# Performance work log

Measured on AMD Instinct MI355X. Metric: run time of the kernel, lower is better.

Reference implementation:

```python
import jax, jax.numpy as jnp
import numpy as np

B, N, DIM_IN, DIM_INNER, DIM_OUT, WINDOW = 4, 4096, 1024, 1024, 1024, 128


def setup_inputs() -> dict:
    key = jax.random.key(0)
    k1, k2, k3, k4 = jax.random.split(key, 4)
    x = jax.random.normal(k1, (B, N, DIM_IN), dtype=jnp.float32)
    # to_qkv: Linear(dim_in, 3*dim_inner, bias=False); stored as [in, 3*inner] for x @ W
    w_qkv = jax.random.normal(k2, (DIM_IN, 3 * DIM_INNER), dtype=jnp.float32) / np.sqrt(DIM_IN)
    # to_out: Linear(dim_inner, dim_out) with bias
    w_out = jax.random.normal(k3, (DIM_INNER, DIM_OUT), dtype=jnp.float32) / np.sqrt(DIM_INNER)
    b_out = jax.random.normal(k4, (DIM_OUT,), dtype=jnp.float32) * 0.01
    return {"x": x, "w_qkv": w_qkv, "w_out": w_out, "b_out": b_out}


def reference(x, w_qkv, w_out, b_out):
    b, n, _ = x.shape
    w = WINDOW
    scale = DIM_INNER ** (-0.5)
    # n is a multiple of window, so pad_to_multiple is a no-op
    qkv = jnp.einsum('bnd,de->bne', x, w_qkv)
    q, k, v = jnp.split(qkv, 3, axis=-1)
    nw = n // w
    win = lambda t: t.reshape(b, nw, w, DIM_INNER)  # b (w n) d -> b w n d
    q, k, v = win(q), win(k), win(v)
    # pad one zero block at the front of the window axis
    kp = jnp.pad(k, ((0, 0), (1, 0), (0, 0), (0, 0)))
    # concat previous block + current block along token axis -> (b, nw, 2w, d)
    k2 = jnp.concatenate([kp[:, :-1], kp[:, 1:]], axis=2)
    # NOTE: faithful to source bug: the lambda references k (not t), so v is
    # overwritten with the concatenated k blocks as well.
    v2 = k2
    sim = jnp.einsum('bwid,bwjd->bwij', q, k2) * scale  # (b, nw, w, 2w)
    i, j = w, 2 * w
    mask = jnp.triu(jnp.ones((i, j), dtype=bool), j - i + 1)  # causal within lookback window
    mask_value = -jnp.finfo(sim.dtype).max
    sim = jnp.where(mask[None, None], mask_value, sim)
    attn = jax.nn.softmax(sim, axis=-1)
    out = jnp.einsum('bwij,bwjd->bwid', attn, v2)
    out = out.reshape(b, n, DIM_INNER)[:, :n]
    return jnp.einsum('bnd,de->bne', out, w_out) + b_out
```

## Files before the change

### kernel.cpp

```cpp
#include <hip/hip_runtime.h>
#include <float.h>


#define B_SZ 4
#define SEQ 4096
#define DIM 1024
#define WIN 128
#define NWIN 32
#define TW 256
#define NROWS (B_SZ * SEQ)
#define KPAD 4224

typedef float f32x4 __attribute__((ext_vector_type(4)));
typedef __bf16 bf16x8 __attribute__((ext_vector_type(8)));

__device__ __forceinline__ unsigned short f2b(float f) {
    unsigned int u = __float_as_uint(f);
    u += 0x7FFF + ((u >> 16) & 1);
    return (unsigned short)(u >> 16);
}

__device__ __forceinline__ void gld_lds16(const unsigned short* g, unsigned short* l) {
    __builtin_amdgcn_global_load_lds(
        (const __attribute__((address_space(1))) void*)g,
        (__attribute__((address_space(3))) void*)l, 16, 0, 0);
}

__device__ __forceinline__ void mfma_core(
    const unsigned short* __restrict__ A, int lda,
    const unsigned short* __restrict__ Bt, int ldb, int K,
    unsigned short* As, unsigned short* Bs, f32x4 (&acc)[4][4])
{
    const int tid = threadIdx.x;
    const int wv = tid >> 6, lane = tid & 63;
    const int wr = wv >> 1, wc = wv & 1;

#pragma unroll
    for (int m = 0; m < 4; ++m)
#pragma unroll
        for (int n = 0; n < 4; ++n) acc[m][n] = (f32x4){0.f, 0.f, 0.f, 0.f};

    for (int k0 = 0; k0 < K; k0 += 64) {
#pragma unroll
        for (int it = 0; it < 4; ++it) {
            int rbase = wv * 32 + it * 8;
            const unsigned short* g =
                A + (size_t)(rbase + (lane >> 3)) * lda + k0 + (lane & 7) * 8;
            gld_lds16(g, As + rbase * 64);
        }
#pragma unroll
        for (int it = 0; it < 4; ++it) {
            int rbase = wv * 32 + it * 8;
            const unsigned short* g =
                Bt + (size_t)(rbase + (lane >> 3)) * ldb + k0 + (lane & 7) * 8;
            gld_lds16(g, Bs + rbase * 64);
        }
        __syncthreads();

#pragma unroll
        for (int ks = 0; ks < 2; ++ks) {
            bf16x8 af[4], bfr[4];
            const int kof = ks * 32 + (lane >> 4) * 8;
#pragma unroll
            for (int m = 0; m < 4; ++m)
                af[m] = *(const bf16x8*)(As + (wr * 64 + m * 16 + (lane & 15)) * 64 + kof);
#pragma unroll
            for (int n = 0; n < 4; ++n)
                bfr[n] = *(const bf16x8*)(Bs + (wc * 64 + n * 16 + (lane & 15)) * 64 + kof);
#pragma unroll
            for (int m = 0; m < 4; ++m)
#pragma unroll
                for (int n = 0; n < 4; ++n)
                    acc[m][n] = __builtin_amdgcn_mfma_f32_16x16x32_bf16(
                        af[m], bfr[n], acc[m][n], 0, 0, 0);
        }
        __syncthreads();
    }
}


__global__ __launch_bounds__(256) void k_prep_x(const float* __restrict__ x,
                                                unsigned short* __restrict__ xb)
{
    int i = blockIdx.x * 256 + threadIdx.x;
    float4 a = *(const float4*)&x[(size_t)i * 8];
    float4 b = *(const float4*)&x[(size_t)i * 8 + 4];
    ushort4 lo, hi;
    lo.x = f2b(a.x); lo.y = f2b(a.y); lo.z = f2b(a.z); lo.w = f2b(a.w);
    hi.x = f2b(b.x); hi.y = f2b(b.y); hi.z = f2b(b.z); hi.w = f2b(b.w);
    *(ushort4*)&xb[(size_t)i * 8] = lo;
    *(ushort4*)&xb[(size_t)i * 8 + 4] = hi;
}

__global__ __launch_bounds__(256) void k_transpose(const float* __restrict__ src,
    int src_ld, int col0, int R, unsigned short* __restrict__ dst)
{
    __shared__ float T[32][33];
    const int r0 = blockIdx.y * 32, c0 = blockIdx.x * 32;
    const int cx = threadIdx.x & 31, ry = threadIdx.x >> 5;
#pragma unroll
    for (int i = 0; i < 4; ++i)
        T[ry + 8 * i][cx] = src[(size_t)(r0 + ry + 8 * i) * src_ld + col0 + c0 + cx];
    __syncthreads();
#pragma unroll
    for (int i = 0; i < 4; ++i)
        dst[(size_t)(c0 + ry + 8 * i) * R + r0 + cx] = f2b(T[cx][ry + 8 * i]);
}

__global__ __launch_bounds__(256) void k_zero_kpad(unsigned short* __restrict__ kbuf)
{
    int t = blockIdx.x * 256 + threadIdx.x;
    int b = t >> 14, r = t & 16383;
    float4 z = {0.f, 0.f, 0.f, 0.f};
    *(float4*)&kbuf[(size_t)b * KPAD * DIM + (size_t)r * 8] = z;
}

__global__ __launch_bounds__(256) void k_zero_ktpad(unsigned short* __restrict__ ktr)
{
    int t = blockIdx.x * 256 + threadIdx.x;
    int b = t >> 14, rem = t & 16383;
    int d = rem >> 4, s = rem & 15;
    float4 z = {0.f, 0.f, 0.f, 0.f};
    *(float4*)&ktr[((size_t)b * DIM + d) * KPAD + s * 8] = z;
}

__global__ __launch_bounds__(256) void k_gemm_qk(
    const unsigned short* __restrict__ xb, const unsigned short* __restrict__ wqkvT,
    unsigned short* __restrict__ qbuf, unsigned short* __restrict__ kbuf,
    unsigned short* __restrict__ ktr)
{
    __shared__ unsigned short As[128 * 64], Bs[128 * 64];
    f32x4 acc[4][4];
    const int bm = blockIdx.y * 128, bn = blockIdx.x * 128;
    mfma_core(xb + (size_t)bm * DIM, DIM, wqkvT + (size_t)bn * DIM, DIM, DIM, As, Bs, acc);

    const int tid = threadIdx.x, wv = tid >> 6, lane = tid & 63;
    const int wr = wv >> 1, wc = wv & 1;
#pragma unroll
    for (int m = 0; m < 4; ++m) {
        const int row0 = bm + wr * 64 + m * 16 + (lane >> 4) * 4;
#pragma unroll
        for (int n = 0; n < 4; ++n) {
            const int col = bn + wc * 64 + n * 16 + (lane & 15);
            if (col < DIM) {
#pragma unroll
                for (int r = 0; r < 4; ++r)
                    qbuf[(size_t)(row0 + r) * DIM + col] = f2b(acc[m][n][r]);
            } else {
                const int d = col - DIM;
                const int b = row0 >> 12, tok0 = row0 & 4095;
#pragma unroll
                for (int r = 0; r < 4; ++r)
                    kbuf[((size_t)b * KPAD + 128 + tok0 + r) * DIM + d] = f2b(acc[m][n][r]);
                ushort4 kt;
                kt.x = f2b(acc[m][n][0]); kt.y = f2b(acc[m][n][1]);
                kt.z = f2b(acc[m][n][2]); kt.w = f2b(acc[m][n][3]);
                *(ushort4*)&ktr[((size_t)b * DIM + d) * KPAD + 128 + tok0] = kt;
            }
        }
    }
}

__global__ __launch_bounds__(256) void k_sim(
    const unsigned short* __restrict__ qbuf, const unsigned short* __restrict__ kbuf,
    float* __restrict__ sim)
{
    __shared__ unsigned short As[128 * 64], Bs[128 * 64];
    f32x4 acc[4][4];
    const int win = blockIdx.y, ct = blockIdx.x;
    const int b = win >> 5, w = win & 31;
    const unsigned short* Ap = qbuf + ((size_t)b * SEQ + w * WIN) * DIM;
    const unsigned short* Bp = kbuf + ((size_t)b * KPAD + w * WIN + ct * 128) * DIM;
    mfma_core(Ap, DIM, Bp, DIM, DIM, As, Bs, acc);

    const int tid = threadIdx.x, wv = tid >> 6, lane = tid & 63;
    const int wr = wv >> 1, wc = wv & 1;
    const float scale = 0.03125f;
#pragma unroll
    for (int m = 0; m < 4; ++m) {
        const int qi0 = wr * 64 + m * 16 + (lane >> 4) * 4;
#pragma unroll
        for (int n = 0; n < 4; ++n) {
            const int jc = ct * 128 + wc * 64 + n * 16 + (lane & 15);
#pragma unroll
            for (int r = 0; r < 4; ++r) {
                const int qi = qi0 + r;
                float v = (jc > qi + WIN) ? -FLT_MAX : acc[m][n][r] * scale;
                sim[((size_t)win * WIN + qi) * TW + jc] = v;
            }
        }
    }
}

__global__ __launch_bounds__(256) void k_softmax(const float* __restrict__ sim,
                                                 unsigned short* __restrict__ attnb)
{
    const int row = blockIdx.x * 4 + (threadIdx.x >> 6);
    const int lane = threadIdx.x & 63;
    const float* p = sim + (size_t)row * TW;
    float4 v = *(const float4*)&p[lane * 4];
    float m = fmaxf(fmaxf(v.x, v.y), fmaxf(v.z, v.w));
#pragma unroll
    for (int off = 32; off; off >>= 1) m = fmaxf(m, __shfl_xor(m, off));
    float e0 = expf(v.x - m), e1 = expf(v.y - m);
    float e2 = expf(v.z - m), e3 = expf(v.w - m);
    float s = e0 + e1 + e2 + e3;
#pragma unroll
    for (int off = 32; off; off >>= 1) s += __shfl_xor(s, off);
    float inv = 1.f / s;
    ushort4 o;
    o.x = f2b(e0 * inv); o.y = f2b(e1 * inv); o.z = f2b(e2 * inv); o.w = f2b(e3 * inv);
    *(ushort4*)&attnb[(size_t)row * TW + lane * 4] = o;
}

__global__ __launch_bounds__(256) void k_pv(
    const unsigned short* __restrict__ attnb, const unsigned short* __restrict__ ktr,
    unsigned short* __restrict__ aout)
{
    __shared__ unsigned short As[128 * 64], Bs[128 * 64];
    f32x4 acc[4][4];
    const int win = blockIdx.y, ct = blockIdx.x;
    const int b = win >> 5, w = win & 31;
    const unsigned short* Ap = attnb + (size_t)win * WIN * TW;
    const unsigned short* Bp = ktr + ((size_t)b * DIM + ct * 128) * KPAD + w * WIN;
    mfma_core(Ap, TW, Bp, KPAD, TW, As, Bs, acc);

    const int tid = threadIdx.x, wv = tid >> 6, lane = tid & 63;
    const int wr = wv >> 1, wc = wv & 1;
#pragma unroll
    for (int m = 0; m < 4; ++m) {
        const int row0 = wr * 64 + m * 16 + (lane >> 4) * 4;
#pragma unroll
        for (int n = 0; n < 4; ++n) {
            const int col = ct * 128 + wc * 64 + n * 16 + (lane & 15);
#pragma unroll
            for (int r = 0; r < 4; ++r)
                aout[((size_t)b * SEQ + w * WIN + row0 + r) * DIM + col] =
                    f2b(acc[m][n][r]);
        }
    }
}

__global__ __launch_bounds__(256) void k_out(
    const unsigned short* __restrict__ aout, const unsigned short* __restrict__ woutT,
    const float* __restrict__ bias, float* __restrict__ out)
{
    __shared__ unsigned short As[128 * 64], Bs[128 * 64];
    f32x4 acc[4][4];
    const int bm = blockIdx.y * 128, bn = blockIdx.x * 128;
    mfma_core(aout + (size_t)bm * DIM, DIM, woutT + (size_t)bn * DIM, DIM, DIM, As, Bs, acc);

    const int tid = threadIdx.x, wv = tid >> 6, lane = tid & 63;
    const int wr = wv >> 1, wc = wv & 1;
#pragma unroll
    for (int m = 0; m < 4; ++m) {
        const int row0 = bm + wr * 64 + m * 16 + (lane >> 4) * 4;
#pragma unroll
        for (int n = 0; n < 4; ++n) {
            const int col = bn + wc * 64 + n * 16 + (lane & 15);
            const float bb = bias[col];
#pragma unroll
            for (int r = 0; r < 4; ++r)
                out[(size_t)(row0 + r) * DIM + col] = acc[m][n][r] + bb;
        }
    }
}

extern "C" void kernel_launch(void* const* d_in, const int* in_sizes, int n_in,
                              void* d_out, int out_size, void* d_ws, size_t ws_size,
                              hipStream_t stream)
{
    const float* x     = (const float*)d_in[0];
    const float* w_qkv = (const float*)d_in[1];
    const float* w_out = (const float*)d_in[2];
    const float* b_out = (const float*)d_in[3];
    float* out = (float*)d_out;

    char* p = (char*)d_ws;
    unsigned short* xb    = (unsigned short*)p; p += (size_t)NROWS * DIM * 2;
    unsigned short* wqkvT = (unsigned short*)p; p += (size_t)2 * DIM * DIM * 2;
    unsigned short* woutT = (unsigned short*)p; p += (size_t)DIM * DIM * 2;
    unsigned short* qbuf  = (unsigned short*)p; p += (size_t)NROWS * DIM * 2;
    unsigned short* kbuf  = (unsigned short*)p; p += (size_t)B_SZ * KPAD * DIM * 2;
    unsigned short* ktr   = (unsigned short*)p; p += (size_t)B_SZ * DIM * KPAD * 2;
    float*          simb  = (float*)p;          p += (size_t)NROWS * TW * 4;
    unsigned short* attnb = (unsigned short*)p; p += (size_t)NROWS * TW * 2;
    unsigned short* aout  = (unsigned short*)p; p += (size_t)NROWS * DIM * 2;

    k_prep_x<<<NROWS * DIM / 8 / 256, 256, 0, stream>>>(x, xb);
    k_transpose<<<dim3(2 * DIM / 32, DIM / 32), 256, 0, stream>>>(w_qkv, 3 * DIM, 0, DIM, wqkvT);
    k_transpose<<<dim3(DIM / 32, DIM / 32), 256, 0, stream>>>(w_out, DIM, 0, DIM, woutT);
    k_zero_kpad<<<256, 256, 0, stream>>>(kbuf);
    k_zero_ktpad<<<256, 256, 0, stream>>>(ktr);

    k_gemm_qk<<<dim3(2 * DIM / 128, NROWS / 128), 256, 0, stream>>>(xb, wqkvT, qbuf, kbuf, ktr);
    k_sim<<<dim3(2, B_SZ * NWIN), 256, 0, stream>>>(qbuf, kbuf, simb);
    k_softmax<<<NROWS / 4, 256, 0, stream>>>(simb, attnb);
    k_pv<<<dim3(DIM / 128, B_SZ * NWIN), 256, 0, stream>>>(attnb, ktr, aout);
    k_out<<<dim3(DIM / 128, NROWS / 128), 256, 0, stream>>>(aout, woutT, b_out, out);
}
```

Measured before the change: 364.9 us.

## Use 256x256 double-buffered swizzled MFMA GEMM core for QK and output projections

Adds a new GEMM core that uses 256x256 output tiles with 512 threads, double-buffered LDS filled by direct global-to-LDS loads, XOR-swizzled LDS reads and a phased schedule with explicit waitcnt, barriers and s_setprio. The QK projection and the output projection kernels move to it, with a remapped 1D grid that groups tiles for cache locality. The aim is more data reuse per tile and overlap of global loads with MFMA work in the two largest GEMMs. The cost is 128KB of LDS and a large accumulator per block, which limits occupancy and relies on the hand-tuned wait counts being correct.

```diff
diff --git a/kernel.cpp b/kernel.cpp
--- a/kernel.cpp
+++ b/kernel.cpp
@@ -26,6 +26,114 @@
         (__attribute__((address_space(3))) void*)l, 16, 0, 0);
 }
 
+__device__ __forceinline__ bf16x8 lds_read_swz(const unsigned short* tb, int row, int kbyte) {
+    int L = row * 128 + kbyte;
+    L ^= ((L >> 9) & 1) << 5;
+    return *(const bf16x8*)((const char*)tb + L);
+}
+
+#define BAR __builtin_amdgcn_s_barrier()
+#define PRI1 __builtin_amdgcn_s_setprio(1)
+#define PRI0 __builtin_amdgcn_s_setprio(0)
+#define WAIT_LGKM0 do { asm volatile("s_waitcnt lgkmcnt(0)" ::: "memory"); \
+                        __builtin_amdgcn_sched_barrier(0); } while (0)
+#define WAIT_VM8   do { asm volatile("s_waitcnt vmcnt(8)" ::: "memory");  \
+                        __builtin_amdgcn_sched_barrier(0); } while (0)
+#define WAIT_VM0   do { asm volatile("s_waitcnt vmcnt(0)" ::: "memory");  \
+                        __builtin_amdgcn_sched_barrier(0); } while (0)
+
+#define LDAF(BUF, MH)                                                        \
+    _Pragma("unroll") for (int m_ = 0; m_ < 4; ++m_)                         \
+    _Pragma("unroll") for (int ks_ = 0; ks_ < 2; ++ks_)                      \
+        afq[MH][m_][ks_] = lds_read_swz(bufA[BUF],                           \
+            wr * 128 + (MH) * 64 + m_ * 16 + fr, ks_ * 64 + kby);
+
+#define LDBF(BUF, NH)                                                        \
+    _Pragma("unroll") for (int n_ = 0; n_ < 2; ++n_)                         \
+    _Pragma("unroll") for (int ks_ = 0; ks_ < 2; ++ks_)                      \
+        bfq[n_][ks_] = lds_read_swz(bufB[BUF],                               \
+            wc * 64 + (NH) * 32 + n_ * 16 + fr, ks_ * 64 + kby);
+
+#define MFQ(MH, NH)                                                          \
+    _Pragma("unroll") for (int ks_ = 0; ks_ < 2; ++ks_)                      \
+    _Pragma("unroll") for (int m_ = 0; m_ < 4; ++m_)                         \
+    _Pragma("unroll") for (int n_ = 0; n_ < 2; ++n_)                         \
+        acc[(MH) * 4 + m_][(NH) * 2 + n_] =                                  \
+            __builtin_amdgcn_mfma_f32_16x16x32_bf16(afq[MH][m_][ks_],        \
+                bfq[n_][ks_], acc[(MH) * 4 + m_][(NH) * 2 + n_], 0, 0, 0);
+
+#define STG_A(BUF, HJ, K0) gld_lds16(A + soffA[HJ] + (K0), bufA[BUF] + ldst[HJ])
+#define STG_B(BUF, HJ, K0) gld_lds16(Bt + soffB[HJ] + (K0), bufB[BUF] + ldst[HJ])
+
+#define PHASES03(BUF, KST, ST)                                               \
+    LDAF(BUF, 0); LDBF(BUF, 0);                                              \
+    BAR; WAIT_LGKM0; PRI1; MFQ(0, 0); PRI0; BAR;                             \
+    LDAF(BUF, 1);                                                            \
+    BAR; WAIT_LGKM0; PRI1; MFQ(1, 0); PRI0; BAR;                             \
+    LDBF(BUF, 1);                                                            \
+    if (ST) { STG_A(BUF, 0, KST); STG_A(BUF, 1, KST);                        \
+              STG_A(BUF, 2, KST); STG_A(BUF, 3, KST); }                      \
+    BAR; WAIT_LGKM0; PRI1; MFQ(1, 1); PRI0; BAR;                             \
+    if (ST) { STG_B(BUF, 0, KST); STG_B(BUF, 1, KST);                        \
+              STG_B(BUF, 2, KST); STG_B(BUF, 3, KST); }                      \
+    BAR; WAIT_LGKM0; PRI1; MFQ(0, 1); PRI0;
+
+__device__ __forceinline__ void core256(
+    const unsigned short* __restrict__ A, int lda,
+    const unsigned short* __restrict__ Bt, int ldb, int K,
+    unsigned short* lds, f32x4 (&acc)[8][4],
+    int wid, int lane, int wr, int wc)
+{
+    unsigned short* bufA[2] = { lds, lds + 32768 };
+    unsigned short* bufB[2] = { lds + 16384, lds + 49152 };
+
+    const int kby = (lane >> 4) * 16;
+    const int fr = lane & 15;
+
+    int soffA[4], soffB[4], ldst[4];
+#pragma unroll
+    for (int hj = 0; hj < 4; ++hj) {
+        const int half = hj >> 1, j = hj & 1;
+        const int P = half * 16384 + wid * 2048 + j * 1024 + lane * 16;
+        const int L = P ^ (((P >> 9) & 1) << 5);
+        const int row = L >> 7, col = (L & 127) >> 1;
+        soffA[hj] = row * lda + col;
+        soffB[hj] = row * ldb + col;
+        ldst[hj] = (half * 16384 + wid * 2048 + j * 1024) >> 1;
+    }
+
+    bf16x8 afq[2][4][2], bfq[2][2];
+#pragma unroll
+    for (int m = 0; m < 8; ++m)
+#pragma unroll
+        for (int n = 0; n < 4; ++n) acc[m][n] = (f32x4){0.f, 0.f, 0.f, 0.f};
+
+#pragma unroll
+    for (int hj = 0; hj < 4; ++hj) STG_A(0, hj, 0);
+#pragma unroll
+    for (int hj = 0; hj < 4; ++hj) STG_B(0, hj, 0);
+#pragma unroll
+    for (int hj = 0; hj < 4; ++hj) STG_A(1, hj, 64);
+#pragma unroll
+    for (int hj = 0; hj < 4; ++hj) STG_B(1, hj, 64);
+    WAIT_VM8;
+    BAR;
+
+    const int NITER = K >> 7;
+#pragma unroll 1
+    for (int i = 0; i < NITER; ++i) {
+        const bool st = (i + 1 < NITER);
+        const int ka = (2 * i + 2) * 64;
+        const int kb = (2 * i + 3) * 64;
+        PHASES03(0, ka, st)
+        if (st) { WAIT_VM8; } else { WAIT_VM0; }
+        BAR;
+        PHASES03(1, kb, st)
+        if (st) { WAIT_VM8; }
+        BAR;
+    }
+}
+
 __device__ __forceinline__ void mfma_core(
     const unsigned short* __restrict__ A, int lda,
     const unsigned short* __restrict__ Bt, int ldb, int K,
@@ -77,7 +185,6 @@
         __syncthreads();
     }
 }
-
 
 __global__ __launch_bounds__(256) void k_prep_x(const float* __restrict__ x,
                                                 unsigned short* __restrict__ xb)
@@ -124,24 +231,30 @@
     *(float4*)&ktr[((size_t)b * DIM + d) * KPAD + s * 8] = z;
 }
 
-__global__ __launch_bounds__(256) void k_gemm_qk(
+__global__ __launch_bounds__(512, 2) void k_gemm_qk(
     const unsigned short* __restrict__ xb, const unsigned short* __restrict__ wqkvT,
     unsigned short* __restrict__ qbuf, unsigned short* __restrict__ kbuf,
     unsigned short* __restrict__ ktr)
 {
-    __shared__ unsigned short As[128 * 64], Bs[128 * 64];
-    f32x4 acc[4][4];
-    const int bm = blockIdx.y * 128, bn = blockIdx.x * 128;
-    mfma_core(xb + (size_t)bm * DIM, DIM, wqkvT + (size_t)bn * DIM, DIM, DIM, As, Bs, acc);
-
-    const int tid = threadIdx.x, wv = tid >> 6, lane = tid & 63;
-    const int wr = wv >> 1, wc = wv & 1;
-#pragma unroll
-    for (int m = 0; m < 4; ++m) {
-        const int row0 = bm + wr * 64 + m * 16 + (lane >> 4) * 4;
+    __shared__ unsigned short lds[65536];
+    const int tid = threadIdx.x, wid = tid >> 6, lane = tid & 63;
+    const int wr = wid >> 2, wc = wid & 3;
+    const int wg = blockIdx.x;
+    const int x = (wg & 7) * 64 + (wg >> 3);
+    const int bm = (x & 63) * 256;
+    const int bn = (x >> 6) * 256;
+
+    f32x4 acc[8][4];
+    core256(xb + (size_t)bm * DIM, DIM, wqkvT + (size_t)bn * DIM, DIM, DIM,
+            lds, acc, wid, lane, wr, wc);
+
+    const int fr = lane & 15;
+#pragma unroll
+    for (int m = 0; m < 8; ++m) {
+        const int row0 = bm + wr * 128 + m * 16 + (lane >> 4) * 4;
 #pragma unroll
         for (int n = 0; n < 4; ++n) {
-            const int col = bn + wc * 64 + n * 16 + (lane & 15);
+            const int col = bn + wc * 64 + n * 16 + fr;
             if (col < DIM) {
 #pragma unroll
                 for (int r = 0; r < 4; ++r)
@@ -161,6 +274,37 @@
     }
 }
 
+__global__ __launch_bounds__(512, 2) void k_out(
+    const unsigned short* __restrict__ aout, const unsigned short* __restrict__ woutT,
+    const float* __restrict__ bias, float* __restrict__ out)
+{
+    __shared__ unsigned short lds[65536];
+    const int tid = threadIdx.x, wid = tid >> 6, lane = tid & 63;
+    const int wr = wid >> 2, wc = wid & 3;
+    const int wg = blockIdx.x;
+    const int x = (wg & 7) * 32 + (wg >> 3);
+    const int bm = (x & 63) * 256;
+    const int bn = (x >> 6) * 256;
+
+    f32x4 acc[8][4];
+    core256(aout + (size_t)bm * DIM, DIM, woutT + (size_t)bn * DIM, DIM, DIM,
+            lds, acc, wid, lane, wr, wc);
+
+    const int fr = lane & 15;
+#pragma unroll
+    for (int m = 0; m < 8; ++m) {
+        const int row0 = bm + wr * 128 + m * 16 + (lane >> 4) * 4;
+#pragma unroll
+        for (int n = 0; n < 4; ++n) {
+            const int col = bn + wc * 64 + n * 16 + fr;
+            const float bb = bias[col];
+#pragma unroll
+            for (int r = 0; r < 4; ++r)
+                out[(size_t)(row0 + r) * DIM + col] = acc[m][n][r] + bb;
+        }
+    }
+}
+
 __global__ __launch_bounds__(256) void k_sim(
     const unsigned short* __restrict__ qbuf, const unsigned short* __restrict__ kbuf,
     float* __restrict__ sim)
@@ -237,31 +381,6 @@
             for (int r = 0; r < 4; ++r)
                 aout[((size_t)b * SEQ + w * WIN + row0 + r) * DIM + col] =
                     f2b(acc[m][n][r]);
-        }
-    }
-}
-
-__global__ __launch_bounds__(256) void k_out(
-    const unsigned short* __restrict__ aout, const unsigned short* __restrict__ woutT,
-    const float* __restrict__ bias, float* __restrict__ out)
-{
-    __shared__ unsigned short As[128 * 64], Bs[128 * 64];
-    f32x4 acc[4][4];
-    const int bm = blockIdx.y * 128, bn = blockIdx.x * 128;
-    mfma_core(aout + (size_t)bm * DIM, DIM, woutT + (size_t)bn * DIM, DIM, DIM, As, Bs, acc);
-
-    const int tid = threadIdx.x, wv = tid >> 6, lane = tid & 63;
-    const int wr = wv >> 1, wc = wv & 1;
-#pragma unroll
-    for (int m = 0; m < 4; ++m) {
-        const int row0 = bm + wr * 64 + m * 16 + (lane >> 4) * 4;
-#pragma unroll
-        for (int n = 0; n < 4; ++n) {
-            const int col = bn + wc * 64 + n * 16 + (lane & 15);
-            const float bb = bias[col];
-#pragma unroll
-            for (int r = 0; r < 4; ++r)
-                out[(size_t)(row0 + r) * DIM + col] = acc[m][n][r] + bb;
         }
     }
 }
@@ -293,9 +412,9 @@
     k_zero_kpad<<<256, 256, 0, stream>>>(kbuf);
     k_zero_ktpad<<<256, 256, 0, stream>>>(ktr);
 
-    k_gemm_qk<<<dim3(2 * DIM / 128, NROWS / 128), 256, 0, stream>>>(xb, wqkvT, qbuf, kbuf, ktr);
+    k_gemm_qk<<<512, 512, 0, stream>>>(xb, wqkvT, qbuf, kbuf, ktr);
     k_sim<<<dim3(2, B_SZ * NWIN), 256, 0, stream>>>(qbuf, kbuf, simb);
     k_softmax<<<NROWS / 4, 256, 0, stream>>>(simb, attnb);
     k_pv<<<dim3(DIM / 128, B_SZ * NWIN), 256, 0, stream>>>(attnb, ktr, aout);
-    k_out<<<dim3(DIM / 128, NROWS / 128), 256, 0, stream>>>(aout, woutT, b_out, out);
-}
+    k_out<<<256, 512, 0, stream>>>(aout, woutT, b_out, out);
+}
```

Result: slower. 380.7 us (+4.3%).
